# Optimization experiments

Measured on AMD Instinct MI355X. Metric: run time of the kernel, lower is better.

The kernel has to match this reference:

```python
import jax, jax.numpy as jnp
import numpy as np

PI = 3.141592653589793


def setup_inputs() -> dict:
    key = jax.random.key(0)
    ks = jax.random.split(key, 6)
    N, M, D, H = 2048, 512, 2, 128
    inp = {
        "input": jax.random.uniform(ks[0], (N, D), dtype=jnp.float32),
        "quad_x": jax.random.uniform(ks[1], (M, D), dtype=jnp.float32),
        "eq_param": jax.random.uniform(ks[2], (1,), dtype=jnp.float32),
        "W1": jax.random.normal(ks[3], (2 * D, H), dtype=jnp.float32) / np.sqrt(2 * D),
        "b1": jnp.zeros((H,), dtype=jnp.float32),
        "W2": jax.random.normal(ks[4], (H, H), dtype=jnp.float32) / np.sqrt(H),
        "b2": jnp.zeros((H,), dtype=jnp.float32),
        "W3": jax.random.normal(ks[5], (H, 1), dtype=jnp.float32) / np.sqrt(H),
        "b3": jnp.zeros((1,), dtype=jnp.float32),
    }
    return inp


def reference(input, quad_x, eq_param, W1, b1, W2, b2, W3, b3):
    # r_func: separable sinusoidal source weight per quadrature point -> [M]
    y = jnp.prod(jnp.sin(PI * eq_param * quad_x), axis=1)
    N, D = input.shape
    M = quad_x.shape[0]
    # batched concat over all (i, j) pairs: [N, M, 2D]
    pairs = jnp.concatenate(
        [jnp.broadcast_to(input[:, None, :], (N, M, D)),
         jnp.broadcast_to(quad_x[None, :, :], (N, M, D))], axis=-1)
    h = jnp.tanh(pairs @ W1 + b1)          # [N, M, H]
    h = jnp.tanh(h @ W2 + b2)              # [N, M, H]
    g = (h @ W3 + b3)[..., 0]              # [N, M] scalar mlp output per pair
    out = jnp.sum(g * y[None, :], axis=1, keepdims=True)  # quadrature-weighted sum -> [N, 1]
    return out
```

## Files before the change

kernel.cpp:

```cpp
#include <hip/hip_runtime.h>
#include <hip/hip_bf16.h>


using short8 = __attribute__((ext_vector_type(8))) short;
using f32x4  = __attribute__((ext_vector_type(4))) float;

#define N_IN   2048
#define M_Q    512
#define H_DIM  128
#define JC     32
#define JCHUNK 16

#define WS_A_OFF     0x000000u
#define WS_B_OFF     0x100000u
#define WS_Y_OFF     0x140000u
#define WS_SUMY_OFF  0x140800u
#define WS_W2T_OFF   0x141000u
#define WS_SP_OFF    0x150000u

#define PI_F   3.14159265358979323846f
#define TSCALE 2.885390081777927f

__device__ __forceinline__ float tanh_pre(float xs) {
    float t = __builtin_amdgcn_exp2f(xs);
    float r = __builtin_amdgcn_rcpf(1.0f + t);
    return __builtin_fmaf(-2.0f, r, 1.0f);
}

__device__ __forceinline__ unsigned short bf16b(float f) {
    __hip_bfloat16 h = __float2bfloat16(f);
    unsigned short u;
    __builtin_memcpy(&u, &h, 2);
    return u;
}

__device__ __forceinline__ void conv8(const float4& a0, const float4& a1,
                                      const float4& b0, const float4& b1,
                                      short8& dst) {
    dst[0] = (short)bf16b(tanh_pre(a0.x + b0.x));
    dst[1] = (short)bf16b(tanh_pre(a0.y + b0.y));
    dst[2] = (short)bf16b(tanh_pre(a0.z + b0.z));
    dst[3] = (short)bf16b(tanh_pre(a0.w + b0.w));
    dst[4] = (short)bf16b(tanh_pre(a1.x + b1.x));
    dst[5] = (short)bf16b(tanh_pre(a1.y + b1.y));
    dst[6] = (short)bf16b(tanh_pre(a1.z + b1.z));
    dst[7] = (short)bf16b(tanh_pre(a1.w + b1.w));
}

__global__ void k_pre(const float* __restrict__ input, const float* __restrict__ qx,
                      const float* __restrict__ eq, const float* __restrict__ W1,
                      const float* __restrict__ b1, const float* __restrict__ W2,
                      float* __restrict__ ws) {
    int b = blockIdx.x, t = threadIdx.x;
    float* A = ws + (WS_A_OFF >> 2);
    float* B = ws + (WS_B_OFF >> 2);
    float* Y = ws + (WS_Y_OFF >> 2);
    unsigned short* W2T = (unsigned short*)((char*)ws + WS_W2T_OFF);

    if (b < 256) {
        int u = b * 256 + t;
#pragma unroll
        for (int rep = 0; rep < 4; ++rep) {
            int idx = u + rep * 65536;
            int i = idx >> 7, h = idx & 127;
            A[idx] = TSCALE * (input[2 * i] * W1[h] + input[2 * i + 1] * W1[128 + h]);
        }
        {
            int j = u >> 7, h = u & 127;
            B[u] = TSCALE * (qx[2 * j] * W1[256 + h] + qx[2 * j + 1] * W1[384 + h] + b1[h]);
        }
        if (u < 16384) {
            int n = u >> 7, k = u & 127;
            W2T[u] = bf16b(TSCALE * W2[k * 128 + n]);
        }
    } else {
        float e = eq[0];
        float s = 0.f;
#pragma unroll
        for (int rep = 0; rep < 2; ++rep) {
            int j = t + rep * 256;
            float yv = sinf(PI_F * e * qx[2 * j]) * sinf(PI_F * e * qx[2 * j + 1]);
            Y[j] = yv;
            s += yv;
        }
        __shared__ float red[4];
        for (int off = 32; off; off >>= 1) s += __shfl_down(s, off);
        if ((t & 63) == 0) red[t >> 6] = s;
        __syncthreads();
        if (t == 0) ws[WS_SUMY_OFF >> 2] = red[0] + red[1] + red[2] + red[3];
    }
}

__global__ __launch_bounds__(256, 2)
void k_main(const float* __restrict__ A, const float* __restrict__ B,
            const float* __restrict__ Y, const unsigned short* __restrict__ W2T,
            const float* __restrict__ b2, const float* __restrict__ W3,
            float* __restrict__ Sp) {
    __shared__ unsigned short W2s[128 * 128];
    __shared__ float Bs[JCHUNK * 128];
    __shared__ float ys[JCHUNK];

    int t = threadIdx.x;
    int wave = t >> 6, lane = t & 63;
    int l16 = lane & 15, lg = lane >> 4;
    int i0 = blockIdx.x * 64 + wave * 16;
    int jbase = blockIdx.y * JCHUNK;

    for (int c = t; c < 2048; c += 256) {
        int n = c >> 4, cb = c & 15;
        short8 v = *(const short8*)(W2T + c * 8);
        int dst = n * 128 + ((((cb * 16) ^ ((n & 7) << 4))) >> 1);
        *(short8*)&W2s[dst] = v;
    }
    for (int o4 = t; o4 < (JCHUNK * 128) >> 2; o4 += 256)
        *(float4*)&Bs[o4 * 4] = *(const float4*)&B[jbase * 128 + o4 * 4];
    if (t < JCHUNK) ys[t] = Y[jbase + t];

    float4 aa[4][2];
#pragma unroll
    for (int kc = 0; kc < 4; ++kc) {
        const float* pa = &A[(i0 + l16) * 128 + kc * 32 + lg * 8];
        aa[kc][0] = *(const float4*)pa;
        aa[kc][1] = *(const float4*)(pa + 4);
    }

    float b2v[8];
#pragma unroll
    for (int nb = 0; nb < 8; ++nb) b2v[nb] = TSCALE * b2[nb * 16 + l16];

    int colb[4];
#pragma unroll
    for (int kc = 0; kc < 4; ++kc)
        colb[kc] = (kc * 64 + lg * 16) ^ ((l16 & 7) << 4);
    const char* wbase = (const char*)W2s + l16 * 256;

    __syncthreads();

    f32x4 acc[8] = {};

#pragma unroll 1
    for (int jj = 0; jj < JCHUNK; ++jj) {
        f32x4 o[8];
#pragma unroll
        for (int nb = 0; nb < 8; ++nb) {
            o[nb][0] = b2v[nb]; o[nb][1] = b2v[nb];
            o[nb][2] = b2v[nb]; o[nb][3] = b2v[nb];
        }

#pragma unroll
        for (int kc = 0; kc < 4; ++kc) {
            const float* bp = &Bs[jj * 128 + kc * 32 + lg * 8];
            float4 bj0 = *(const float4*)bp;
            float4 bj1 = *(const float4*)(bp + 4);
            short8 av;
            conv8(aa[kc][0], aa[kc][1], bj0, bj1, av);
#pragma unroll
            for (int nb = 0; nb < 8; ++nb) {
                short8 wf = *(const short8*)(wbase + nb * 4096 + colb[kc]);
                o[nb] = __builtin_amdgcn_mfma_f32_16x16x32_bf16(av, wf, o[nb], 0, 0, 0);
            }
        }

        float yj = ys[jj];
#pragma unroll
        for (int nb = 0; nb < 8; ++nb)
#pragma unroll
            for (int r = 0; r < 4; ++r)
                acc[nb][r] = __builtin_fmaf(yj, tanh_pre(o[nb][r]), acc[nb][r]);
    }

    float w3v[8];
#pragma unroll
    for (int nb = 0; nb < 8; ++nb) w3v[nb] = W3[nb * 16 + l16];

    float s[4];
#pragma unroll
    for (int r = 0; r < 4; ++r) {
        float v = 0.f;
#pragma unroll
        for (int nb = 0; nb < 8; ++nb)
            v = __builtin_fmaf(acc[nb][r], w3v[nb], v);
        s[r] = v;
    }
#pragma unroll
    for (int m = 1; m < 16; m <<= 1)
#pragma unroll
        for (int r = 0; r < 4; ++r)
            s[r] += __shfl_xor(s[r], m);

    if (l16 == 0) {
        float* dst = Sp + blockIdx.y * N_IN;
#pragma unroll
        for (int r = 0; r < 4; ++r)
            dst[i0 + lg * 4 + r] = s[r];
    }
}

__global__ void k_fin(const float* __restrict__ Sp, const float* __restrict__ b3,
                      const float* __restrict__ ws, float* __restrict__ out) {
    int i = blockIdx.x * 256 + threadIdx.x;
    float acc = b3[0] * ws[WS_SUMY_OFF >> 2];
#pragma unroll
    for (int s = 0; s < JC; ++s) acc += Sp[s * N_IN + i];
    out[i] = acc;
}

extern "C" void kernel_launch(void* const* d_in, const int* in_sizes, int n_in,
                              void* d_out, int out_size, void* d_ws, size_t ws_size,
                              hipStream_t stream) {
    const float* input = (const float*)d_in[0];
    const float* qx    = (const float*)d_in[1];
    const float* eq    = (const float*)d_in[2];
    const float* W1    = (const float*)d_in[3];
    const float* b1    = (const float*)d_in[4];
    const float* W2    = (const float*)d_in[5];
    const float* b2    = (const float*)d_in[6];
    const float* W3    = (const float*)d_in[7];
    const float* b3    = (const float*)d_in[8];
    float* out = (float*)d_out;
    float* ws  = (float*)d_ws;

    const float* A = ws + (WS_A_OFF >> 2);
    const float* B = ws + (WS_B_OFF >> 2);
    const float* Y = ws + (WS_Y_OFF >> 2);
    const unsigned short* W2T = (const unsigned short*)((char*)d_ws + WS_W2T_OFF);
    float* Sp = (float*)((char*)d_ws + WS_SP_OFF);

    k_pre<<<257, 256, 0, stream>>>(input, qx, eq, W1, b1, W2, ws);
    k_main<<<dim3(32, JC), 256, 0, stream>>>(A, B, Y, W2T, b2, W3, Sp);
    k_fin<<<8, 256, 0, stream>>>(Sp, b3, ws, out);
}
```

Baseline: 91.29 us.

## Hold W2 fragments in registers, switch to fp16 MFMA with packed conversion

Drops the shared-memory copy of W2. Each lane now loads its 32 half8 W2 fragments straight into registers, so the inner loop issues no LDS reads for weights. The operand type changes from bf16 to fp16, using the packed round-toward-zero conversion (cvt_pkrtz) in place of per-element bf16 rounding. W3 and y are folded into a per-iteration scalar accumulator, which replaces the 32-register acc array. The cost is about 128 extra VGPRs per thread, which puts pressure on the launch bound of 2 blocks, and fp16 range and precision differ from bf16.

Result: slower. 96.29 us (+5.5%).

```diff
diff --git a/kernel.cpp b/kernel.cpp
--- a/kernel.cpp
+++ b/kernel.cpp
@@ -1,8 +1,10 @@
 #include <hip/hip_runtime.h>
 #include <hip/hip_bf16.h>
-
-
-using short8 = __attribute__((ext_vector_type(8))) short;
+#include <hip/hip_fp16.h>
+
+
+using fp16x2 = __attribute__((ext_vector_type(2))) __fp16;
+using half8  = __attribute__((ext_vector_type(8))) _Float16;
 using f32x4  = __attribute__((ext_vector_type(4))) float;
 
 #define N_IN   2048
@@ -27,24 +29,19 @@
     return __builtin_fmaf(-2.0f, r, 1.0f);
 }
 
-__device__ __forceinline__ unsigned short bf16b(float f) {
-    __hip_bfloat16 h = __float2bfloat16(f);
-    unsigned short u;
-    __builtin_memcpy(&u, &h, 2);
-    return u;
-}
-
 __device__ __forceinline__ void conv8(const float4& a0, const float4& a1,
                                       const float4& b0, const float4& b1,
-                                      short8& dst) {
-    dst[0] = (short)bf16b(tanh_pre(a0.x + b0.x));
-    dst[1] = (short)bf16b(tanh_pre(a0.y + b0.y));
-    dst[2] = (short)bf16b(tanh_pre(a0.z + b0.z));
-    dst[3] = (short)bf16b(tanh_pre(a0.w + b0.w));
-    dst[4] = (short)bf16b(tanh_pre(a1.x + b1.x));
-    dst[5] = (short)bf16b(tanh_pre(a1.y + b1.y));
-    dst[6] = (short)bf16b(tanh_pre(a1.z + b1.z));
-    dst[7] = (short)bf16b(tanh_pre(a1.w + b1.w));
+                                      half8& dst) {
+    float t0 = tanh_pre(a0.x + b0.x), t1 = tanh_pre(a0.y + b0.y);
+    float t2 = tanh_pre(a0.z + b0.z), t3 = tanh_pre(a0.w + b0.w);
+    float t4 = tanh_pre(a1.x + b1.x), t5 = tanh_pre(a1.y + b1.y);
+    float t6 = tanh_pre(a1.z + b1.z), t7 = tanh_pre(a1.w + b1.w);
+    fp16x2 p[4];
+    p[0] = __builtin_amdgcn_cvt_pkrtz(t0, t1);
+    p[1] = __builtin_amdgcn_cvt_pkrtz(t2, t3);
+    p[2] = __builtin_amdgcn_cvt_pkrtz(t4, t5);
+    p[3] = __builtin_amdgcn_cvt_pkrtz(t6, t7);
+    __builtin_memcpy(&dst, p, 16);
 }
 
 __global__ void k_pre(const float* __restrict__ input, const float* __restrict__ qx,
@@ -55,7 +52,7 @@
     float* A = ws + (WS_A_OFF >> 2);
     float* B = ws + (WS_B_OFF >> 2);
     float* Y = ws + (WS_Y_OFF >> 2);
-    unsigned short* W2T = (unsigned short*)((char*)ws + WS_W2T_OFF);
+    _Float16* W2T = (_Float16*)((char*)ws + WS_W2T_OFF);
 
     if (b < 256) {
         int u = b * 256 + t;
@@ -71,7 +68,7 @@
         }
         if (u < 16384) {
             int n = u >> 7, k = u & 127;
-            W2T[u] = bf16b(TSCALE * W2[k * 128 + n]);
+            W2T[u] = (_Float16)(TSCALE * W2[k * 128 + n]);
         }
     } else {
         float e = eq[0];
@@ -93,10 +90,9 @@
 
 __global__ __launch_bounds__(256, 2)
 void k_main(const float* __restrict__ A, const float* __restrict__ B,
-            const float* __restrict__ Y, const unsigned short* __restrict__ W2T,
+            const float* __restrict__ Y, const _Float16* __restrict__ W2T,
             const float* __restrict__ b2, const float* __restrict__ W3,
             float* __restrict__ Sp) {
-    __shared__ unsigned short W2s[128 * 128];
     __shared__ float Bs[JCHUNK * 128];
     __shared__ float ys[JCHUNK];
 
@@ -106,12 +102,6 @@
     int i0 = blockIdx.x * 64 + wave * 16;
     int jbase = blockIdx.y * JCHUNK;
 
-    for (int c = t; c < 2048; c += 256) {
-        int n = c >> 4, cb = c & 15;
-        short8 v = *(const short8*)(W2T + c * 8);
-        int dst = n * 128 + ((((cb * 16) ^ ((n & 7) << 4))) >> 1);
-        *(short8*)&W2s[dst] = v;
-    }
     for (int o4 = t; o4 < (JCHUNK * 128) >> 2; o4 += 256)
         *(float4*)&Bs[o4 * 4] = *(const float4*)&B[jbase * 128 + o4 * 4];
     if (t < JCHUNK) ys[t] = Y[jbase + t];
@@ -124,64 +114,59 @@
         aa[kc][1] = *(const float4*)(pa + 4);
     }
 
-    float b2v[8];
-#pragma unroll
-    for (int nb = 0; nb < 8; ++nb) b2v[nb] = TSCALE * b2[nb * 16 + l16];
-
-    int colb[4];
-#pragma unroll
-    for (int kc = 0; kc < 4; ++kc)
-        colb[kc] = (kc * 64 + lg * 16) ^ ((l16 & 7) << 4);
-    const char* wbase = (const char*)W2s + l16 * 256;
+    half8 wf[8][4];
+#pragma unroll
+    for (int nb = 0; nb < 8; ++nb)
+#pragma unroll
+        for (int kc = 0; kc < 4; ++kc)
+            wf[nb][kc] = *(const half8*)&W2T[(nb * 16 + l16) * 128 + kc * 32 + lg * 8];
+
+    float b2v[8], w3v[8];
+#pragma unroll
+    for (int nb = 0; nb < 8; ++nb) {
+        b2v[nb] = TSCALE * b2[nb * 16 + l16];
+        w3v[nb] = W3[nb * 16 + l16];
+    }
 
     __syncthreads();
 
-    f32x4 acc[8] = {};
+    float s[4] = {};
 
 #pragma unroll 1
     for (int jj = 0; jj < JCHUNK; ++jj) {
-        f32x4 o[8];
-#pragma unroll
-        for (int nb = 0; nb < 8; ++nb) {
-            o[nb][0] = b2v[nb]; o[nb][1] = b2v[nb];
-            o[nb][2] = b2v[nb]; o[nb][3] = b2v[nb];
-        }
-
+        half8 av[4];
 #pragma unroll
         for (int kc = 0; kc < 4; ++kc) {
             const float* bp = &Bs[jj * 128 + kc * 32 + lg * 8];
             float4 bj0 = *(const float4*)bp;
             float4 bj1 = *(const float4*)(bp + 4);
-            short8 av;
-            conv8(aa[kc][0], aa[kc][1], bj0, bj1, av);
-#pragma unroll
-            for (int nb = 0; nb < 8; ++nb) {
-                short8 wf = *(const short8*)(wbase + nb * 4096 + colb[kc]);
-                o[nb] = __builtin_amdgcn_mfma_f32_16x16x32_bf16(av, wf, o[nb], 0, 0, 0);
-            }
-        }
+            conv8(aa[kc][0], aa[kc][1], bj0, bj1, av[kc]);
+        }
+
+        f32x4 o[8];
+#pragma unroll
+        for (int nb = 0; nb < 8; ++nb) {
+            o[nb][0] = b2v[nb]; o[nb][1] = b2v[nb];
+            o[nb][2] = b2v[nb]; o[nb][3] = b2v[nb];
+        }
+#pragma unroll
+        for (int kc = 0; kc < 4; ++kc)
+#pragma unroll
+            for (int nb = 0; nb < 8; ++nb)
+                o[nb] = __builtin_amdgcn_mfma_f32_16x16x32_f16(
+                    av[kc], wf[nb][kc], o[nb], 0, 0, 0);
 
         float yj = ys[jj];
+        float wy[8];
+#pragma unroll
+        for (int nb = 0; nb < 8; ++nb) wy[nb] = w3v[nb] * yj;
 #pragma unroll
         for (int nb = 0; nb < 8; ++nb)
 #pragma unroll
             for (int r = 0; r < 4; ++r)
-                acc[nb][r] = __builtin_fmaf(yj, tanh_pre(o[nb][r]), acc[nb][r]);
-    }
-
-    float w3v[8];
-#pragma unroll
-    for (int nb = 0; nb < 8; ++nb) w3v[nb] = W3[nb * 16 + l16];
-
-    float s[4];
-#pragma unroll
-    for (int r = 0; r < 4; ++r) {
-        float v = 0.f;
-#pragma unroll
-        for (int nb = 0; nb < 8; ++nb)
-            v = __builtin_fmaf(acc[nb][r], w3v[nb], v);
-        s[r] = v;
-    }
+                s[r] = __builtin_fmaf(tanh_pre(o[nb][r]), wy[nb], s[r]);
+    }
+
 #pragma unroll
     for (int m = 1; m < 16; m <<= 1)
 #pragma unroll
@@ -223,7 +208,7 @@
     const float* A = ws + (WS_A_OFF >> 2);
     const float* B = ws + (WS_B_OFF >> 2);
     const float* Y = ws + (WS_Y_OFF >> 2);
-    const unsigned short* W2T = (const unsigned short*)((char*)d_ws + WS_W2T_OFF);
+    const _Float16* W2T = (const _Float16*)((char*)d_ws + WS_W2T_OFF);
     float* Sp = (float*)((char*)d_ws + WS_SP_OFF);
 
     k_pre<<<257, 256, 0, stream>>>(input, qx, eq, W1, b1, W2, ws);
```
